# Performance work log

Hardware: AMD Instinct MI355X
Metric: run time of the kernel (lower is better)

The kernel has to match this reference:

```python
import jax, jax.numpy as jnp
import numpy as np

ALPHA = 0.2      # LeakyReLU negative slope
NEG_INF = -9e15  # mask value from the original code

def setup_inputs() -> dict:
    key = jax.random.key(0)
    k1, k2, k3, k4 = jax.random.split(key, 4)
    B, M, F_IN, F_OUT = 16, 2048, 128, 64
    h = jax.random.normal(k1, (B, M, F_IN), dtype=jnp.float32)
    adj = jax.random.randint(k2, (B, M, M), 0, 2, dtype=jnp.int32)
    W = jax.random.normal(k3, (F_IN, F_OUT), dtype=jnp.float32) * 0.1
    a = jax.random.normal(k4, (2 * F_OUT, 1), dtype=jnp.float32) * 0.1
    return {"h": h, "adj": adj, "W": W, "a": a}

def reference(h, adj, W, a):
    # h: [B,M,Fin], adj: [B,M,M], W: [Fin,E], a: [2E,1]
    Wh = jnp.matmul(h, W)                      # [B,M,E]
    E = Wh.shape[-1]
    a1, a2 = a[:E, 0], a[E:, 0]
    # decompose a^T [Wh_i || Wh_j] = (Wh_i . a1) + (Wh_j . a2)
    f1 = Wh @ a1                               # [B,M] (source/query term)
    f2 = Wh @ a2                               # [B,M] (target/key term)
    e = jax.nn.leaky_relu(f1[:, :, None] + f2[:, None, :], negative_slope=ALPHA)  # [B,M,M]
    scores = jnp.where(adj > 0, e, NEG_INF)
    attn = jax.nn.softmax(scores, axis=-1)     # [B,M,M]  (dropout p=0 / eval mode)
    h_prime = jnp.matmul(attn, Wh)             # [B,M,E]
    return jax.nn.elu(h_prime)                 # concat=True branch
```

## Files before the change

kernel.cpp:

```cpp
#include <hip/hip_runtime.h>


#define M_     2048
#define FIN_   128
#define F_     64
#define ALPHA_ 0.2f
#define ROWS_  32
#define TS_    36
#define WT_    132

typedef float  float4_ __attribute__((ext_vector_type(4)));
typedef short  short4_ __attribute__((ext_vector_type(4)));
typedef short  short8  __attribute__((ext_vector_type(8)));
typedef int    int4_   __attribute__((ext_vector_type(4)));
typedef unsigned short u16;
typedef unsigned int   u32;

static __device__ __forceinline__ float bf2f(u16 u) {
    return __uint_as_float(((u32)u) << 16);
}
static __device__ __forceinline__ u16 f2bf(float f) {
    u32 u = __float_as_uint(f);
    u32 r = u + 0x7FFFu + ((u >> 16) & 1u);
    return (u16)(r >> 16);
}

__global__ __launch_bounds__(256, 4) void k_gat2(
    const float* __restrict__ h, const int* __restrict__ adj,
    const float* __restrict__ W, const float* __restrict__ a,
    float* __restrict__ out)
{
    __shared__ u16   Wl[FIN_ * F_];
    __shared__ float a_s[2 * F_];
    __shared__ float wa1[FIN_], wa2[FIN_];
    __shared__ float f1s[ROWS_];
    __shared__ float dens[ROWS_];
    __shared__ char  dyn[32 * WT_ * 4];

    u16*   hT   = (u16*)dyn;
    u16*   P    = (u16*)(dyn + 9216);
    float* f2t  = (float*)(dyn + 11520);
    float* Tsum = (float*)dyn;

    const int tid  = threadIdx.x;
    const int w    = tid >> 6;
    const int l    = tid & 63;
    const int lc   = l & 15;
    const int quad = l >> 4;
    const int b    = blockIdx.x >> 6;
    const int i0   = (blockIdx.x & 63) * ROWS_;

    if (tid < 128) a_s[tid] = a[tid];
    for (int e = tid; e < FIN_ * F_; e += 256) Wl[e] = f2bf(W[e]);
    __syncthreads();

    if (tid < FIN_) {
        float s1 = 0.f, s2 = 0.f;
#pragma unroll 8
        for (int n = 0; n < F_; ++n) {
            float wv = W[tid * F_ + n];
            s1 += wv * a_s[n];
            s2 += wv * a_s[F_ + n];
        }
        wa1[tid] = s1;
        wa2[tid] = s2;
    }
    __syncthreads();

    {
        const int i = tid >> 3, sub = tid & 7, k0 = sub * 16;
        const float* hp = h + ((size_t)(b * M_ + i0 + i)) * FIN_ + k0;
        float s = 0.f;
#pragma unroll
        for (int k = 0; k < 16; ++k) s += hp[k] * wa1[k0 + k];
        s += __shfl_xor(s, 1, 64);
        s += __shfl_xor(s, 2, 64);
        s += __shfl_xor(s, 4, 64);
        if (sub == 0) f1s[i] = s;
    }
    __syncthreads();

    const int prow = tid >> 3;
    const int ps   = tid & 7;
    const int sf0  = (tid & 15) * 8;
    const int stp  = (tid >> 4) * 2;
    const int mt   = w & 1;
    const int ntb  = (w >> 1) * 4;
    const float f1r = f1s[prow];
    float denacc = 0.f;

    float4_ acc[4];
#pragma unroll
    for (int c = 0; c < 4; ++c) acc[c] = (float4_){0.f, 0.f, 0.f, 0.f};

    const int*   aprow = adj + ((size_t)(b * M_ + i0 + prow)) * M_ + ps * 4;
    const float* hbase = h + ((size_t)(b * M_ + stp)) * FIN_ + sf0;

    for (int it = 0; it < 64; ++it) {
        const int j0 = it * 32;

        int4_ c4 = *(const int4_*)(aprow + j0);

        {
            const float* hp0 = hbase + (size_t)j0 * FIN_;
            const float* hp1 = hp0 + FIN_;
            float4_ x0 = *(const float4_*)hp0, x1 = *(const float4_*)(hp0 + 4);
            float4_ y0 = *(const float4_*)hp1, y1 = *(const float4_*)(hp1 + 4);
            float xa[8] = {x0[0], x0[1], x0[2], x0[3], x1[0], x1[1], x1[2], x1[3]};
            float ya[8] = {y0[0], y0[1], y0[2], y0[3], y1[0], y1[1], y1[2], y1[3]};
            float fp0 = 0.f, fp1 = 0.f;
#pragma unroll
            for (int kk = 0; kk < 8; ++kk) {
                const int k = sf0 + kk;
                u16 u0 = f2bf(xa[kk]), u1 = f2bf(ya[kk]);
                *(u32*)(hT + k * TS_ + stp) = (u32)u0 | ((u32)u1 << 16);
                fp0 += xa[kk] * wa2[k];
                fp1 += ya[kk] * wa2[k];
            }
            fp0 += __shfl_xor(fp0, 1, 64); fp1 += __shfl_xor(fp1, 1, 64);
            fp0 += __shfl_xor(fp0, 2, 64); fp1 += __shfl_xor(fp1, 2, 64);
            fp0 += __shfl_xor(fp0, 4, 64); fp1 += __shfl_xor(fp1, 4, 64);
            fp0 += __shfl_xor(fp0, 8, 64); fp1 += __shfl_xor(fp1, 8, 64);
            if ((tid & 15) == 0) { f2t[stp] = fp0; f2t[stp + 1] = fp1; }
        }
        __syncthreads();

        {
            float4_ g = *(const float4_*)(f2t + ps * 4);
            u32 pk0, pk1;
            float d = 0.f;
            {
                float x_ = f1r + g[0]; x_ = fmaxf(x_, ALPHA_ * x_);
                float e_ = (c4[0] > 0) ? __expf(x_) : 0.f;
                u16 pb = f2bf(e_); d += bf2f(pb); pk0 = (u32)pb;
            }
            {
                float x_ = f1r + g[1]; x_ = fmaxf(x_, ALPHA_ * x_);
                float e_ = (c4[1] > 0) ? __expf(x_) : 0.f;
                u16 pb = f2bf(e_); d += bf2f(pb); pk0 |= ((u32)pb << 16);
            }
            {
                float x_ = f1r + g[2]; x_ = fmaxf(x_, ALPHA_ * x_);
                float e_ = (c4[2] > 0) ? __expf(x_) : 0.f;
                u16 pb = f2bf(e_); d += bf2f(pb); pk1 = (u32)pb;
            }
            {
                float x_ = f1r + g[3]; x_ = fmaxf(x_, ALPHA_ * x_);
                float e_ = (c4[3] > 0) ? __expf(x_) : 0.f;
                u16 pb = f2bf(e_); d += bf2f(pb); pk1 |= ((u32)pb << 16);
            }
            *(u32*)(P + prow * TS_ + ps * 4)     = pk0;
            *(u32*)(P + prow * TS_ + ps * 4 + 2) = pk1;
            denacc += d;
        }
        __syncthreads();

        {
            const u16* apx = P + (mt * 16 + lc) * TS_ + quad * 8;
            short4_ a0 = *(const short4_*)apx;
            short4_ a1 = *(const short4_*)(apx + 4);
            short8 af;
            af[0] = a0[0]; af[1] = a0[1]; af[2] = a0[2]; af[3] = a0[3];
            af[4] = a1[0]; af[5] = a1[1]; af[6] = a1[2]; af[7] = a1[3];
#pragma unroll
            for (int c = 0; c < 4; ++c) {
                const u16* bp = hT + ((ntb + c) * 16 + lc) * TS_ + quad * 8;
                short4_ b0 = *(const short4_*)bp;
                short4_ b1 = *(const short4_*)(bp + 4);
                short8 bf;
                bf[0] = b0[0]; bf[1] = b0[1]; bf[2] = b0[2]; bf[3] = b0[3];
                bf[4] = b1[0]; bf[5] = b1[1]; bf[6] = b1[2]; bf[7] = b1[3];
                acc[c] = __builtin_amdgcn_mfma_f32_16x16x32_bf16(af, bf, acc[c], 0, 0, 0);
            }
        }
        __syncthreads();
    }

    denacc += __shfl_xor(denacc, 1, 64);
    denacc += __shfl_xor(denacc, 2, 64);
    denacc += __shfl_xor(denacc, 4, 64);
    if (ps == 0) dens[prow] = denacc;

#pragma unroll
    for (int c = 0; c < 4; ++c)
#pragma unroll
        for (int mm = 0; mm < 4; ++mm)
            Tsum[(mt * 16 + quad * 4 + mm) * WT_ + (ntb + c) * 16 + lc] = acc[c][mm];
    __syncthreads();

    {
        const int row = tid >> 3;
        const int n0  = (tid & 7) * 8;
        const float den  = dens[row];
        const float rden = (den > 0.f) ? (1.f / den) : 0.f;
        float u[8];
#pragma unroll
        for (int nn = 0; nn < 8; ++nn) u[nn] = 0.f;
        for (int k = 0; k < FIN_; ++k) {
            const float tv = Tsum[row * WT_ + k];
            const u16* wp = &Wl[k * F_ + n0];
#pragma unroll
            for (int nn = 0; nn < 8; ++nn) u[nn] += tv * bf2f(wp[nn]);
        }
        float4_ o0, o1;
#pragma unroll
        for (int nn = 0; nn < 8; ++nn) {
            float hp = u[nn] * rden;
            float o  = hp > 0.f ? hp : expm1f(hp);
            if (nn < 4) o0[nn] = o; else o1[nn - 4] = o;
        }
        float* op = out + ((size_t)(b * M_ + i0 + row)) * F_ + n0;
        *(float4_*)op       = o0;
        *(float4_*)(op + 4) = o1;
    }
}

extern "C" void kernel_launch(void* const* d_in, const int* in_sizes, int n_in,
                              void* d_out, int out_size, void* d_ws, size_t ws_size,
                              hipStream_t stream)
{
    (void)out_size; (void)d_ws; (void)ws_size;
    const float* h  = (const float*)d_in[0];
    const int* adjp = (const int*)d_in[1];
    const float* Wp = (const float*)d_in[2];
    const float* ap = (const float*)d_in[3];
    for (int i = 0; i < n_in; ++i) {
        long s = in_sizes[i];
        if      (s == 4194304L)  h    = (const float*)d_in[i];
        else if (s == 67108864L) adjp = (const int*)d_in[i];
        else if (s == 8192L)     Wp   = (const float*)d_in[i];
        else if (s == 128L)      ap   = (const float*)d_in[i];
    }
    k_gat2<<<1024, 256, 0, stream>>>(h, adjp, Wp, ap, (float*)d_out);
}
```

Measured before the change: 433.5 us.

## Precompute Wh and attention logits in a prepass, simplify attention kernel

Adds a prepass kernel that computes Wh = hW in bf16 (stored transposed in the workspace) along with the f1/f2 logit terms. A new attention kernel then streams adj and WhT straight into MFMA registers with no shared-memory staging and no per-iteration barriers. This removes the repeated per-block recomputation of h projections and the trailing W multiply. The cost is an extra launch and workspace traffic, and the fused kernel remains as a fallback when no workspace is available.

```diff
diff --git a/kernel.cpp b/kernel.cpp
--- a/kernel.cpp
+++ b/kernel.cpp
@@ -5,9 +5,6 @@
 #define FIN_   128
 #define F_     64
 #define ALPHA_ 0.2f
-#define ROWS_  32
-#define TS_    36
-#define WT_    132
 
 typedef float  float4_ __attribute__((ext_vector_type(4)));
 typedef short  short4_ __attribute__((ext_vector_type(4)));
@@ -24,6 +21,122 @@
     u32 r = u + 0x7FFFu + ((u >> 16) & 1u);
     return (u16)(r >> 16);
 }
+
+
+__global__ __launch_bounds__(256) void k_pre(
+    const float* __restrict__ h, const float* __restrict__ W,
+    const float* __restrict__ a, u16* __restrict__ WhT,
+    float* __restrict__ f1, float* __restrict__ f2)
+{
+    const int row = blockIdx.x * 4 + (threadIdx.x >> 6);
+    const int n   = threadIdx.x & 63;
+
+    float acc = 0.f;
+    const float* hp = h + (size_t)row * FIN_;
+    for (int k = 0; k < FIN_; ++k)
+        acc += hp[k] * W[k * F_ + n];
+
+    const int b = row >> 11, jm = row & 2047;
+    WhT[((size_t)b * F_ + n) * M_ + jm] = f2bf(acc);
+
+    float s1 = acc * a[n], s2 = acc * a[F_ + n];
+#pragma unroll
+    for (int off = 1; off < 64; off <<= 1) {
+        s1 += __shfl_xor(s1, off, 64);
+        s2 += __shfl_xor(s2, off, 64);
+    }
+    if (n == 0) { f1[row] = s1; f2[row] = s2; }
+}
+
+__global__ __launch_bounds__(256, 4) void k_attn2(
+    const int* __restrict__ adj, const u16* __restrict__ WhT,
+    const float* __restrict__ f1, const float* __restrict__ f2,
+    float* __restrict__ out)
+{
+    __shared__ float f2s[M_];
+    __shared__ float f1s[32];
+    __shared__ float dens[32];
+
+    const int tid  = threadIdx.x;
+    const int w    = tid >> 6;
+    const int l    = tid & 63;
+    const int lc   = l & 15;
+    const int quad = l >> 4;
+    const int b    = blockIdx.x >> 6;
+    const int i0   = (blockIdx.x & 63) * 32;
+    const int mt   = w & 1;
+    const int ntp  = w >> 1;
+
+    {
+        const float4_* src = (const float4_*)(f2 + b * M_);
+        float4_* dst = (float4_*)f2s;
+        for (int i = tid; i < M_ / 4; i += 256) dst[i] = src[i];
+    }
+    if (tid < 32) f1s[tid] = f1[b * M_ + i0 + tid];
+    __syncthreads();
+
+    const float f1r = f1s[mt * 16 + lc];
+    const int*  ap  = adj + ((size_t)(b * M_ + i0 + mt * 16 + lc)) * M_ + quad * 8;
+    const u16*  wp0 = WhT + (size_t)b * F_ * M_ + (size_t)(ntp * 32 + lc) * M_ + quad * 8;
+    const u16*  wp1 = wp0 + (size_t)16 * M_;
+    const float* fp = f2s + quad * 8;
+
+    float4_ acc0 = (float4_){0.f, 0.f, 0.f, 0.f};
+    float4_ acc1 = (float4_){0.f, 0.f, 0.f, 0.f};
+    float dsum = 0.f;
+
+    for (int it = 0; it < 64; ++it) {
+        const int j0 = it * 32;
+        int4_   c0 = *(const int4_*)(ap + j0);
+        int4_   c1 = *(const int4_*)(ap + j0 + 4);
+        float4_ g0 = *(const float4_*)(fp + j0);
+        float4_ g1 = *(const float4_*)(fp + j0 + 4);
+
+        short8 af;
+        float d = 0.f;
+#define GAT_SC(jj, ai, gi)                                          \
+        {                                                           \
+            float x_ = f1r + (gi);                                  \
+            x_ = fmaxf(x_, ALPHA_ * x_);                            \
+            float e_ = ((ai) > 0) ? __expf(x_) : 0.f;               \
+            u16 pb_ = f2bf(e_);                                     \
+            af[jj] = (short)pb_;                                    \
+            d += bf2f(pb_);                                         \
+        }
+        GAT_SC(0, c0[0], g0[0]) GAT_SC(1, c0[1], g0[1])
+        GAT_SC(2, c0[2], g0[2]) GAT_SC(3, c0[3], g0[3])
+        GAT_SC(4, c1[0], g1[0]) GAT_SC(5, c1[1], g1[1])
+        GAT_SC(6, c1[2], g1[2]) GAT_SC(7, c1[3], g1[3])
+#undef GAT_SC
+        dsum += d;
+
+        short8 b0 = *(const short8*)(wp0 + j0);
+        short8 b1 = *(const short8*)(wp1 + j0);
+        acc0 = __builtin_amdgcn_mfma_f32_16x16x32_bf16(af, b0, acc0, 0, 0, 0);
+        acc1 = __builtin_amdgcn_mfma_f32_16x16x32_bf16(af, b1, acc1, 0, 0, 0);
+    }
+
+    dsum += __shfl_xor(dsum, 16, 64);
+    dsum += __shfl_xor(dsum, 32, 64);
+    if (w < 2 && l < 16) dens[mt * 16 + l] = dsum;
+    __syncthreads();
+
+#pragma unroll
+    for (int mm = 0; mm < 4; ++mm) {
+        const int rr  = mt * 16 + quad * 4 + mm;
+        const float den  = dens[rr];
+        const float rden = (den > 0.f) ? (1.f / den) : 0.f;
+        float* op = out + ((size_t)(b * M_ + i0 + rr)) * F_ + ntp * 32 + lc;
+        float v0 = acc0[mm] * rden;
+        float v1 = acc1[mm] * rden;
+        op[0]  = v0 > 0.f ? v0 : expm1f(v0);
+        op[16] = v1 > 0.f ? v1 : expm1f(v1);
+    }
+}
+
+#define ROWS_  32
+#define TS_    36
+#define WT_    132
 
 __global__ __launch_bounds__(256, 4) void k_gat2(
     const float* __restrict__ h, const int* __restrict__ adj,
@@ -98,9 +211,7 @@
 
     for (int it = 0; it < 64; ++it) {
         const int j0 = it * 32;
-
         int4_ c4 = *(const int4_*)(aprow + j0);
-
         {
             const float* hp0 = hbase + (size_t)j0 * FIN_;
             const float* hp1 = hp0 + FIN_;
@@ -124,7 +235,6 @@
             if ((tid & 15) == 0) { f2t[stp] = fp0; f2t[stp + 1] = fp1; }
         }
         __syncthreads();
-
         {
             float4_ g = *(const float4_*)(f2t + ps * 4);
             u32 pk0, pk1;
@@ -154,7 +264,6 @@
             denacc += d;
         }
         __syncthreads();
-
         {
             const u16* apx = P + (mt * 16 + lc) * TS_ + quad * 8;
             short4_ a0 = *(const short4_*)apx;
@@ -198,15 +307,15 @@
         for (int nn = 0; nn < 8; ++nn) u[nn] = 0.f;
         for (int k = 0; k < FIN_; ++k) {
             const float tv = Tsum[row * WT_ + k];
-            const u16* wp = &Wl[k * F_ + n0];
-#pragma unroll
-            for (int nn = 0; nn < 8; ++nn) u[nn] += tv * bf2f(wp[nn]);
+            const u16* wq = &Wl[k * F_ + n0];
+#pragma unroll
+            for (int nn = 0; nn < 8; ++nn) u[nn] += tv * bf2f(wq[nn]);
         }
         float4_ o0, o1;
 #pragma unroll
         for (int nn = 0; nn < 8; ++nn) {
-            float hp = u[nn] * rden;
-            float o  = hp > 0.f ? hp : expm1f(hp);
+            float hv = u[nn] * rden;
+            float o  = hv > 0.f ? hv : expm1f(hv);
             if (nn < 4) o0[nn] = o; else o1[nn - 4] = o;
         }
         float* op = out + ((size_t)(b * M_ + i0 + row)) * F_ + n0;
@@ -219,7 +328,7 @@
                               void* d_out, int out_size, void* d_ws, size_t ws_size,
                               hipStream_t stream)
 {
-    (void)out_size; (void)d_ws; (void)ws_size;
+    (void)out_size;
     const float* h  = (const float*)d_in[0];
     const int* adjp = (const int*)d_in[1];
     const float* Wp = (const float*)d_in[2];
@@ -231,5 +340,17 @@
         else if (s == 8192L)     Wp   = (const float*)d_in[i];
         else if (s == 128L)      ap   = (const float*)d_in[i];
     }
-    k_gat2<<<1024, 256, 0, stream>>>(h, adjp, Wp, ap, (float*)d_out);
-}
+    float* out = (float*)d_out;
+
+    const size_t NEED = 4194304u + 131072u + 131072u;
+    if (d_ws != nullptr && ws_size >= NEED) {
+        char* ws = (char*)d_ws;
+        u16*   WhT = (u16*)ws;
+        float* f1  = (float*)(ws + 4194304);
+        float* f2  = (float*)(ws + 4194304 + 131072);
+        k_pre  <<<8192, 256, 0, stream>>>(h, Wp, ap, WhT, f1, f2);
+        k_attn2<<<1024, 256, 0, stream>>>(adjp, WhT, f1, f2, out);
+    } else {
+        k_gat2<<<1024, 256, 0, stream>>>(h, adjp, Wp, ap, out);
+    }
+}
```

Result: slower. 510.7 us (+17.8%).
